# Kernel optimization log

Measured on AMD Instinct MI355X. Metric: run time of the kernel, lower is better.

Reference implementation:

```python
import jax, jax.numpy as jnp
import numpy as np

N = 10000      # nodes
E = 320000     # edges (before self-loops)
D_IN = 256
HID = 128
HEADS = 4
D_OUT = 256
SLOPE = 0.2    # PyG GATConv default negative_slope


def setup_inputs() -> dict:
    key = jax.random.key(0)
    ks = jax.random.split(key, 10)
    s = 0.05
    return {
        "x": jax.random.normal(ks[0], (N, D_IN), dtype=jnp.float32),
        "edge_index": jax.random.randint(ks[1], (2, E), 0, N),
        # layer 1: in=256 -> heads=4, out=128, concat
        "W1": jax.random.normal(ks[2], (D_IN, HEADS * HID), dtype=jnp.float32) * s,
        "a1_src": jax.random.normal(ks[3], (HEADS, HID), dtype=jnp.float32) * s,
        "a1_dst": jax.random.normal(ks[4], (HEADS, HID), dtype=jnp.float32) * s,
        "b1": jax.random.normal(ks[5], (HEADS * HID,), dtype=jnp.float32) * s,
        # layer 2: in=512 -> heads=1, out=256, no concat
        "W2": jax.random.normal(ks[6], (HEADS * HID, D_OUT), dtype=jnp.float32) * s,
        "a2_src": jax.random.normal(ks[7], (1, D_OUT), dtype=jnp.float32) * s,
        "a2_dst": jax.random.normal(ks[8], (1, D_OUT), dtype=jnp.float32) * s,
        "b2": jax.random.normal(ks[9], (D_OUT,), dtype=jnp.float32) * s,
    }


def gat_conv(x, src, dst, W, a_src, a_dst, bias, heads, out_dim, concat):
    """PyG-style GATConv (eval mode, self-loops pre-added to src/dst)."""
    n = x.shape[0]
    h = (x @ W).reshape(n, heads, out_dim)            # [N, H, F]
    # per-edge attention logits: LeakyReLU(a_src.h_src + a_dst.h_dst)
    as_n = (h * a_src).sum(-1)                         # [N, H]
    ad_n = (h * a_dst).sum(-1)                         # [N, H]
    logit = jax.nn.leaky_relu(as_n[src] + ad_n[dst], negative_slope=SLOPE)  # [E, H]
    # segment softmax over edges grouped by destination node
    logit = logit - jax.ops.segment_max(logit, dst, num_segments=n)[dst]
    ex = jnp.exp(logit)
    alpha = ex / jax.ops.segment_sum(ex, dst, num_segments=n)[dst]          # [E, H]
    # weighted scatter-aggregation of source messages
    out = jax.ops.segment_sum(h[src] * alpha[:, :, None], dst, num_segments=n)  # [N, H, F]
    out = out.reshape(n, heads * out_dim) if concat else out.mean(axis=1)
    return out + bias


def reference(x, edge_index, W1, a1_src, a1_dst, b1, W2, a2_src, a2_dst, b2):
    # add self-loops once (PyG GATConv default add_self_loops=True)
    loops = jnp.arange(N, dtype=edge_index.dtype)
    src = jnp.concatenate([edge_index[0], loops])
    dst = jnp.concatenate([edge_index[1], loops])
    h = gat_conv(x, src, dst, W1, a1_src, a1_dst, b1, HEADS, HID, True)
    h = jax.nn.elu(h)  # dropout is identity at eval
    return gat_conv(h, src, dst, W2, a2_src, a2_dst, b2, 1, D_OUT, False)
```

## Files before the change

### kernel.cpp

```cpp
#include <hip/hip_runtime.h>

#define N_NODES 10000
#define E_RAW   320000
#define E_TOT   330000
#define D_IN    256
#define HID     128
#define HEADS   4
#define F1      512
#define D_OUT   256
#define SLOPE   0.2f

typedef __attribute__((ext_vector_type(8))) short bf16x8;
typedef __attribute__((ext_vector_type(4))) float f32x4;

__device__ __forceinline__ float bf2f(ushort u) {
    return __uint_as_float(((uint)u) << 16);
}
__device__ __forceinline__ ushort f2bf(float x) {
    uint u = __float_as_uint(x);
    uint r = (u + 0x7FFFu + ((u >> 16) & 1u)) >> 16;
    return (ushort)r;
}
__device__ __forceinline__ float bfu_lo(uint u) { return __uint_as_float(u << 16); }
__device__ __forceinline__ float bfu_hi(uint u) { return __uint_as_float(u & 0xFFFF0000u); }

__device__ __forceinline__ void gload_lds16(const void* g, void* l) {
    __builtin_amdgcn_global_load_lds(
        (const __attribute__((address_space(1))) void*)g,
        (__attribute__((address_space(3))) void*)l, 16, 0, 0);
}


__global__ __launch_bounds__(256) void k_zero(int* __restrict__ p, int n) {
    int i = blockIdx.x * 256 + threadIdx.x;
    if (i < n) p[i] = 0;
}

__global__ __launch_bounds__(256) void k_hist(const int* __restrict__ ei, int* __restrict__ deg) {
    int e = blockIdx.x * 256 + threadIdx.x;
    if (e < E_TOT) {
        int dst = (e < E_RAW) ? ei[E_RAW + e] : (e - E_RAW);
        atomicAdd(&deg[dst], 1);
    }
}

#define SCAN_CHUNK 40

__global__ __launch_bounds__(256) void k_scan(const int* __restrict__ deg,
                                              int* __restrict__ row_start,
                                              int* __restrict__ cursor) {
    __shared__ int tots[256];
    int tid = threadIdx.x;
    int base = tid * SCAN_CHUNK;
    int loc[SCAN_CHUNK];
    int s = 0;
    #pragma unroll
    for (int k = 0; k < SCAN_CHUNK; k++) {
        int idx = base + k;
        int v = (idx < N_NODES) ? deg[idx] : 0;
        loc[k] = s;
        s += v;
    }
    tots[tid] = s;
    __syncthreads();
    for (int off = 1; off < 256; off <<= 1) {
        int t = (tid >= off) ? tots[tid - off] : 0;
        __syncthreads();
        tots[tid] += t;
        __syncthreads();
    }
    int excl = tots[tid] - s;
    #pragma unroll
    for (int k = 0; k < SCAN_CHUNK; k++) {
        int idx = base + k;
        if (idx < N_NODES) {
            int r = excl + loc[k];
            row_start[idx] = r;
            cursor[idx]    = r;
        }
    }
    if (tid == 255) row_start[N_NODES] = E_TOT;
}

__global__ __launch_bounds__(256) void k_scatter(const int* __restrict__ ei,
                                                 int* __restrict__ cursor,
                                                 int* __restrict__ csr_src) {
    int e = blockIdx.x * 256 + threadIdx.x;
    if (e < E_TOT) {
        int src = (e < E_RAW) ? ei[e] : (e - E_RAW);
        int dst = (e < E_RAW) ? ei[E_RAW + e] : (e - E_RAW);
        int pos = atomicAdd(&cursor[dst], 1);
        csr_src[pos] = src;
    }
}


__global__ __launch_bounds__(256) void k_cast8(const float* __restrict__ in,
                                               ushort* __restrict__ outp, int n8) {
    int i = blockIdx.x * 256 + threadIdx.x;
    if (i < n8) {
        float4 a = *(const float4*)&in[(size_t)i * 8];
        float4 b = *(const float4*)&in[(size_t)i * 8 + 4];
        uint4 u;
        u.x = (uint)f2bf(a.x) | ((uint)f2bf(a.y) << 16);
        u.y = (uint)f2bf(a.z) | ((uint)f2bf(a.w) << 16);
        u.z = (uint)f2bf(b.x) | ((uint)f2bf(b.y) << 16);
        u.w = (uint)f2bf(b.z) | ((uint)f2bf(b.w) << 16);
        *(uint4*)&outp[(size_t)i * 8] = u;
    }
}

__global__ __launch_bounds__(256) void k_castT(const float* __restrict__ in,
                                               ushort* __restrict__ outp,
                                               int K, int N) {
    int i = blockIdx.x * 256 + threadIdx.x;
    if (i < K * N) {
        int k = i / N, n = i - k * N;
        outp[(size_t)n * K + k] = f2bf(in[i]);
    }
}


__global__ __launch_bounds__(256) void k_gemm(const ushort* __restrict__ A,
                                              const ushort* __restrict__ B,
                                              ushort* __restrict__ C,
                                              int M, int N, int K) {
    __shared__ ushort sA[128 * 64];
    __shared__ ushort sB[64 * 64];

    const int tid = threadIdx.x;
    const int lane = tid & 63;
    const int wid = tid >> 6;
    const int wr = wid >> 1;
    const int wc = wid & 1;
    const int m0 = blockIdx.y * 128;
    const int n0 = blockIdx.x * 64;
    const int fr = lane & 15;
    const int fs = lane >> 4;

    const int rowc = lane >> 3;
    const int slot = (lane & 7) ^ rowc;

    f32x4 acc[4][2];
    #pragma unroll
    for (int i = 0; i < 4; i++)
        #pragma unroll
        for (int j = 0; j < 2; j++) acc[i][j] = (f32x4){0.f, 0.f, 0.f, 0.f};

    for (int k0 = 0; k0 < K; k0 += 64) {
        #pragma unroll
        for (int t = 0; t < 4; t++) {
            int c = wid + 4 * t;
            int gr = m0 + c * 8 + rowc;
            gr = gr < M ? gr : M - 1;
            gload_lds16(A + (size_t)gr * K + k0 + slot * 8, &sA[c * 512]);
        }
        #pragma unroll
        for (int t = 0; t < 2; t++) {
            int c = wid + 4 * t;
            int gc = n0 + c * 8 + rowc;
            gload_lds16(B + (size_t)gc * K + k0 + slot * 8, &sB[c * 512]);
        }
        __syncthreads();
        #pragma unroll
        for (int kk = 0; kk < 2; kk++) {
            int sbase = kk * 4 + fs;
            bf16x8 a_f[4], b_f[2];
            #pragma unroll
            for (int i = 0; i < 4; i++) {
                int r = wr * 64 + i * 16 + fr;
                a_f[i] = *(const bf16x8*)&sA[r * 64 + ((sbase ^ (r & 7)) << 3)];
            }
            #pragma unroll
            for (int j = 0; j < 2; j++) {
                int cc = wc * 32 + j * 16 + fr;
                b_f[j] = *(const bf16x8*)&sB[cc * 64 + ((sbase ^ (cc & 7)) << 3)];
            }
            #pragma unroll
            for (int i = 0; i < 4; i++)
                #pragma unroll
                for (int j = 0; j < 2; j++)
                    acc[i][j] = __builtin_amdgcn_mfma_f32_16x16x32_bf16(a_f[i], b_f[j], acc[i][j], 0, 0, 0);
        }
        __syncthreads();
    }

    #pragma unroll
    for (int i = 0; i < 4; i++) {
        #pragma unroll
        for (int j = 0; j < 2; j++) {
            int row_base = m0 + wr * 64 + i * 16 + ((lane >> 4) << 2);
            int col = n0 + wc * 32 + j * 16 + (lane & 15);
            #pragma unroll
            for (int q = 0; q < 4; q++) {
                int r = row_base + q;
                if (r < M) C[(size_t)r * N + col] = f2bf(acc[i][j][q]);
            }
        }
    }
}


__global__ __launch_bounds__(256) void k_attn_vec1(const ushort* __restrict__ h1,
                                                   const float* __restrict__ a1s,
                                                   const float* __restrict__ a1d,
                                                   float* __restrict__ as1,
                                                   float* __restrict__ ad1) {
    int node = blockIdx.x * 4 + (threadIdx.x >> 6);
    int lane = threadIdx.x & 63;
    uint4 hv = *(const uint4*)(h1 + (size_t)node * F1 + (size_t)lane * 8);
    const float* sp = a1s + lane * 8;
    const float* dp = a1d + lane * 8;
    float4 sa = *(const float4*)sp, sb = *(const float4*)(sp + 4);
    float4 da = *(const float4*)dp, db = *(const float4*)(dp + 4);
    float h0 = bfu_lo(hv.x), h1v = bfu_hi(hv.x), h2v = bfu_lo(hv.y), h3 = bfu_hi(hv.y);
    float h4 = bfu_lo(hv.z), h5 = bfu_hi(hv.z), h6 = bfu_lo(hv.w), h7 = bfu_hi(hv.w);
    float s_ = h0*sa.x + h1v*sa.y + h2v*sa.z + h3*sa.w + h4*sb.x + h5*sb.y + h6*sb.z + h7*sb.w;
    float d_ = h0*da.x + h1v*da.y + h2v*da.z + h3*da.w + h4*db.x + h5*db.y + h6*db.z + h7*db.w;
    #pragma unroll
    for (int off = 8; off >= 1; off >>= 1) {
        s_ += __shfl_xor(s_, off, 64);
        d_ += __shfl_xor(d_, off, 64);
    }
    if ((lane & 15) == 0) {
        int head = lane >> 4;
        as1[node * 4 + head] = s_;
        ad1[node * 4 + head] = d_;
    }
}

__global__ __launch_bounds__(256) void k_attn_vec2(const ushort* __restrict__ h2,
                                                   const float* __restrict__ a2s,
                                                   const float* __restrict__ a2d,
                                                   float* __restrict__ as2,
                                                   float* __restrict__ ad2) {
    int node = blockIdx.x * 4 + (threadIdx.x >> 6);
    int lane = threadIdx.x & 63;
    uint2 hv = *(const uint2*)(h2 + (size_t)node * D_OUT + lane * 4);
    float h0 = bfu_lo(hv.x), h1v = bfu_hi(hv.x), h2v = bfu_lo(hv.y), h3 = bfu_hi(hv.y);
    float4 sv = *(const float4*)(a2s + lane * 4);
    float4 dv = *(const float4*)(a2d + lane * 4);
    float s_ = h0 * sv.x + h1v * sv.y + h2v * sv.z + h3 * sv.w;
    float d_ = h0 * dv.x + h1v * dv.y + h2v * dv.z + h3 * dv.w;
    #pragma unroll
    for (int off = 32; off >= 1; off >>= 1) {
        s_ += __shfl_xor(s_, off, 64);
        d_ += __shfl_xor(d_, off, 64);
    }
    if (lane == 0) { as2[node] = s_; ad2[node] = d_; }
}


__device__ __forceinline__ void fma8(uint4 v, float e, float* acc) {
    acc[0] += bfu_lo(v.x) * e; acc[1] += bfu_hi(v.x) * e;
    acc[2] += bfu_lo(v.y) * e; acc[3] += bfu_hi(v.y) * e;
    acc[4] += bfu_lo(v.z) * e; acc[5] += bfu_hi(v.z) * e;
    acc[6] += bfu_lo(v.w) * e; acc[7] += bfu_hi(v.w) * e;
}

__global__ __launch_bounds__(256) void k_edge1(const int* __restrict__ row_start,
                                               const int* __restrict__ csr_src,
                                               const ushort* __restrict__ h1,
                                               const float* __restrict__ as1,
                                               const float* __restrict__ ad1,
                                               const float* __restrict__ b1,
                                               ushort* __restrict__ heluh) {
    int node = blockIdx.x * 4 + (threadIdx.x >> 6);
    int lane = threadIdx.x & 63;
    int start = row_start[node];
    int end   = row_start[node + 1];
    int h_lane = lane >> 4;

    float adl = ad1[node * 4 + h_lane];

    float acc[8] = {0,0,0,0,0,0,0,0};
    float sum = 0.f;
    const size_t lo8 = (size_t)lane * 8;

    int i = start;
    for (; i + 8 <= end; i += 8) {
        int s[8];
        #pragma unroll
        for (int k = 0; k < 8; k++) s[k] = csr_src[i + k];
        float l[8];
        #pragma unroll
        for (int k = 0; k < 8; k++) l[k] = as1[s[k] * 4 + h_lane];
        uint4 v[8];
        #pragma unroll
        for (int k = 0; k < 8; k++) v[k] = *(const uint4*)(h1 + (size_t)s[k] * F1 + lo8);
        #pragma unroll
        for (int k = 0; k < 8; k++) {
            float t = l[k] + adl;
            t = t > 0.f ? t : SLOPE * t;
            float e = __expf(t);
            sum += e;
            fma8(v[k], e, acc);
        }
    }
    for (; i < end; i++) {
        int s0 = csr_src[i];
        float t = as1[s0 * 4 + h_lane] + adl;
        uint4 v0 = *(const uint4*)(h1 + (size_t)s0 * F1 + lo8);
        t = t > 0.f ? t : SLOPE * t;
        float e = __expf(t);
        sum += e;
        fma8(v0, e, acc);
    }
    float inv = 1.f / sum;

    size_t o = (size_t)node * F1 + lo8;
    const float* bp = b1 + lo8;
    uint pk[4];
    #pragma unroll
    for (int j = 0; j < 4; j++) {
        float v0 = acc[2*j]   * inv + bp[2*j];
        float v1 = acc[2*j+1] * inv + bp[2*j+1];
        v0 = v0 > 0.f ? v0 : (__expf(v0) - 1.f);
        v1 = v1 > 0.f ? v1 : (__expf(v1) - 1.f);
        pk[j] = (uint)f2bf(v0) | ((uint)f2bf(v1) << 16);
    }
    *(uint4*)&heluh[o] = make_uint4(pk[0], pk[1], pk[2], pk[3]);
}

__global__ __launch_bounds__(256) void k_edge2(const int* __restrict__ row_start,
                                               const int* __restrict__ csr_src,
                                               const ushort* __restrict__ h2,
                                               const float* __restrict__ as2,
                                               const float* __restrict__ ad2,
                                               const float* __restrict__ b2,
                                               float* __restrict__ out) {
    int node = blockIdx.x * 4 + (threadIdx.x >> 6);
    int lane = threadIdx.x & 63;
    int start = row_start[node];
    int end   = row_start[node + 1];

    float ad = ad2[node];

    float acc[4] = {0,0,0,0};
    float sum = 0.f;
    const size_t lo4 = (size_t)lane * 4;

    int i = start;
    for (; i + 8 <= end; i += 8) {
        int s[8];
        #pragma unroll
        for (int k = 0; k < 8; k++) s[k] = csr_src[i + k];
        float l[8];
        #pragma unroll
        for (int k = 0; k < 8; k++) l[k] = as2[s[k]];
        uint2 v[8];
        #pragma unroll
        for (int k = 0; k < 8; k++) v[k] = *(const uint2*)(h2 + (size_t)s[k] * D_OUT + lo4);
        #pragma unroll
        for (int k = 0; k < 8; k++) {
            float t = l[k] + ad;
            t = t > 0.f ? t : SLOPE * t;
            float e = __expf(t);
            sum += e;
            acc[0] += bfu_lo(v[k].x) * e; acc[1] += bfu_hi(v[k].x) * e;
            acc[2] += bfu_lo(v[k].y) * e; acc[3] += bfu_hi(v[k].y) * e;
        }
    }
    for (; i < end; i++) {
        int s0 = csr_src[i];
        float t = as2[s0] + ad;
        uint2 v0 = *(const uint2*)(h2 + (size_t)s0 * D_OUT + lo4);
        t = t > 0.f ? t : SLOPE * t;
        float e = __expf(t);
        sum += e;
        acc[0] += bfu_lo(v0.x) * e; acc[1] += bfu_hi(v0.x) * e;
        acc[2] += bfu_lo(v0.y) * e; acc[3] += bfu_hi(v0.y) * e;
    }
    float inv = 1.f / sum;
    float4 r;
    r.x = acc[0] * inv + b2[lo4 + 0];
    r.y = acc[1] * inv + b2[lo4 + 1];
    r.z = acc[2] * inv + b2[lo4 + 2];
    r.w = acc[3] * inv + b2[lo4 + 3];
    *(float4*)&out[(size_t)node * D_OUT + lo4] = r;
}


extern "C" void kernel_launch(void* const* d_in, const int* in_sizes, int n_in,
                              void* d_out, int out_size, void* d_ws, size_t ws_size,
                              hipStream_t stream) {
    const float* x   = (const float*)d_in[0];
    const int*   ei  = (const int*)d_in[1];
    const float* W1  = (const float*)d_in[2];
    const float* a1s = (const float*)d_in[3];
    const float* a1d = (const float*)d_in[4];
    const float* b1  = (const float*)d_in[5];
    const float* W2  = (const float*)d_in[6];
    const float* a2s = (const float*)d_in[7];
    const float* a2d = (const float*)d_in[8];
    const float* b2  = (const float*)d_in[9];
    float* out = (float*)d_out;

    char* ws = (char*)d_ws;
    size_t off = 0;
    auto take = [&](size_t bytes) {
        char* p = ws + off;
        off += (bytes + 255) & ~(size_t)255;
        return p;
    };
    int*    deg       = (int*)take(sizeof(int) * N_NODES);
    int*    row_start = (int*)take(sizeof(int) * (N_NODES + 1));
    int*    cursor    = (int*)take(sizeof(int) * N_NODES);
    int*    csr_src   = (int*)take(sizeof(int) * E_TOT);
    ushort* xb        = (ushort*)take(sizeof(ushort) * (size_t)N_NODES * D_IN);
    ushort* w1h       = (ushort*)take(sizeof(ushort) * D_IN * F1);
    ushort* w2h       = (ushort*)take(sizeof(ushort) * F1 * D_OUT);
    ushort* h1        = (ushort*)take(sizeof(ushort) * (size_t)N_NODES * F1);
    float*  as1       = (float*)take(sizeof(float) * N_NODES * 4);
    float*  ad1       = (float*)take(sizeof(float) * N_NODES * 4);
    ushort* heluh     = (ushort*)take(sizeof(ushort) * (size_t)N_NODES * F1);
    ushort* h2        = (ushort*)take(sizeof(ushort) * (size_t)N_NODES * D_OUT);
    float*  as2       = (float*)take(sizeof(float) * N_NODES);
    float*  ad2       = (float*)take(sizeof(float) * N_NODES);

    int eblocks = (E_TOT + 255) / 256;
    k_zero<<<(N_NODES + 255) / 256, 256, 0, stream>>>(deg, N_NODES);
    k_hist<<<eblocks, 256, 0, stream>>>(ei, deg);
    k_scan<<<1, 256, 0, stream>>>(deg, row_start, cursor);
    k_scatter<<<eblocks, 256, 0, stream>>>(ei, cursor, csr_src);

    k_cast8<<<(N_NODES * D_IN / 8 + 255) / 256, 256, 0, stream>>>(x, xb, N_NODES * D_IN / 8);
    k_castT<<<(D_IN * F1 + 255) / 256, 256, 0, stream>>>(W1, w1h, D_IN, F1);
    k_castT<<<(F1 * D_OUT + 255) / 256, 256, 0, stream>>>(W2, w2h, F1, D_OUT);

    k_gemm<<<dim3(F1 / 64, (N_NODES + 127) / 128), 256, 0, stream>>>(xb, w1h, h1, N_NODES, F1, D_IN);
    k_attn_vec1<<<N_NODES / 4, 256, 0, stream>>>(h1, a1s, a1d, as1, ad1);
    k_edge1<<<N_NODES / 4, 256, 0, stream>>>(row_start, csr_src, h1, as1, ad1, b1, heluh);

    k_gemm<<<dim3(D_OUT / 64, (N_NODES + 127) / 128), 256, 0, stream>>>(heluh, w2h, h2, N_NODES, D_OUT, F1);
    k_attn_vec2<<<N_NODES / 4, 256, 0, stream>>>(h2, a2s, a2d, as2, ad2);
    k_edge2<<<N_NODES / 4, 256, 0, stream>>>(row_start, csr_src, h2, as2, ad2, b2, out);
}
```

Baseline: 168.1 us.

## Fuse attention-vector dots into GEMM epilogues and merge prep kernels

Computes the per-node attention dot products in the GEMM epilogues with shuffle reductions and atomicAdd, which removes the separate attn_vec kernels and their re-read of h1/h2. The scan and all casts go into one multi-role prep kernel, and the CSR scatter shares a launch with GEMM1 blocks. k_edge2 now has each half-wave take alternate edges with 16-byte loads. Together these cut the launch count, at the cost of extra zeroing and atomic traffic and a float summation order that is no longer deterministic.

```diff
diff --git a/kernel.cpp b/kernel.cpp
--- a/kernel.cpp
+++ b/kernel.cpp
@@ -9,6 +9,7 @@
 #define F1      512
 #define D_OUT   256
 #define SLOPE   0.2f
+#define EBLOCKS 1290
 
 typedef __attribute__((ext_vector_type(8))) short bf16x8;
 typedef __attribute__((ext_vector_type(4))) float f32x4;
@@ -31,10 +32,16 @@
 }
 
 
-__global__ __launch_bounds__(256) void k_zero(int* __restrict__ p, int n) {
+__global__ __launch_bounds__(256) void k_zero_all(int* __restrict__ deg,
+                                                  float* __restrict__ as1,
+                                                  float* __restrict__ ad1,
+                                                  float* __restrict__ as2,
+                                                  float* __restrict__ ad2) {
     int i = blockIdx.x * 256 + threadIdx.x;
-    if (i < n) p[i] = 0;
-}
+    if (i < 4 * N_NODES) { as1[i] = 0.f; ad1[i] = 0.f; }
+    if (i < N_NODES) { deg[i] = 0; as2[i] = 0.f; ad2[i] = 0.f; }
+}
+
 
 __global__ __launch_bounds__(256) void k_hist(const int* __restrict__ ei, int* __restrict__ deg) {
     int e = blockIdx.x * 256 + threadIdx.x;
@@ -44,210 +51,227 @@
     }
 }
 
+
 #define SCAN_CHUNK 40
 
-__global__ __launch_bounds__(256) void k_scan(const int* __restrict__ deg,
+__global__ __launch_bounds__(256) void k_prep(const int* __restrict__ deg,
                                               int* __restrict__ row_start,
-                                              int* __restrict__ cursor) {
-    __shared__ int tots[256];
+                                              int* __restrict__ cursor,
+                                              const float* __restrict__ W1,
+                                              ushort* __restrict__ w1h,
+                                              const float* __restrict__ W2,
+                                              ushort* __restrict__ w2h,
+                                              const float* __restrict__ x,
+                                              ushort* __restrict__ xb) {
+    int b = blockIdx.x;
     int tid = threadIdx.x;
-    int base = tid * SCAN_CHUNK;
-    int loc[SCAN_CHUNK];
-    int s = 0;
-    #pragma unroll
-    for (int k = 0; k < SCAN_CHUNK; k++) {
-        int idx = base + k;
-        int v = (idx < N_NODES) ? deg[idx] : 0;
-        loc[k] = s;
-        s += v;
-    }
-    tots[tid] = s;
-    __syncthreads();
-    for (int off = 1; off < 256; off <<= 1) {
-        int t = (tid >= off) ? tots[tid - off] : 0;
+    if (b == 0) {
+        __shared__ int tots[256];
+        int base = tid * SCAN_CHUNK;
+        int loc[SCAN_CHUNK];
+        int s = 0;
+        #pragma unroll
+        for (int k = 0; k < SCAN_CHUNK; k++) {
+            int idx = base + k;
+            int v = (idx < N_NODES) ? deg[idx] : 0;
+            loc[k] = s;
+            s += v;
+        }
+        tots[tid] = s;
         __syncthreads();
-        tots[tid] += t;
-        __syncthreads();
-    }
-    int excl = tots[tid] - s;
-    #pragma unroll
-    for (int k = 0; k < SCAN_CHUNK; k++) {
-        int idx = base + k;
-        if (idx < N_NODES) {
-            int r = excl + loc[k];
-            row_start[idx] = r;
-            cursor[idx]    = r;
-        }
-    }
-    if (tid == 255) row_start[N_NODES] = E_TOT;
-}
-
-__global__ __launch_bounds__(256) void k_scatter(const int* __restrict__ ei,
-                                                 int* __restrict__ cursor,
-                                                 int* __restrict__ csr_src) {
-    int e = blockIdx.x * 256 + threadIdx.x;
-    if (e < E_TOT) {
-        int src = (e < E_RAW) ? ei[e] : (e - E_RAW);
-        int dst = (e < E_RAW) ? ei[E_RAW + e] : (e - E_RAW);
-        int pos = atomicAdd(&cursor[dst], 1);
-        csr_src[pos] = src;
-    }
-}
-
-
-__global__ __launch_bounds__(256) void k_cast8(const float* __restrict__ in,
-                                               ushort* __restrict__ outp, int n8) {
-    int i = blockIdx.x * 256 + threadIdx.x;
-    if (i < n8) {
-        float4 a = *(const float4*)&in[(size_t)i * 8];
-        float4 b = *(const float4*)&in[(size_t)i * 8 + 4];
+        for (int off = 1; off < 256; off <<= 1) {
+            int t = (tid >= off) ? tots[tid - off] : 0;
+            __syncthreads();
+            tots[tid] += t;
+            __syncthreads();
+        }
+        int excl = tots[tid] - s;
+        #pragma unroll
+        for (int k = 0; k < SCAN_CHUNK; k++) {
+            int idx = base + k;
+            if (idx < N_NODES) {
+                int r = excl + loc[k];
+                row_start[idx] = r;
+                cursor[idx]    = r;
+            }
+        }
+        if (tid == 255) row_start[N_NODES] = E_TOT;
+    } else if (b <= 512) {
+        int i = (b - 1) * 256 + tid;
+        int k = i / F1, n = i - k * F1;
+        w1h[(size_t)n * D_IN + k] = f2bf(W1[i]);
+    } else if (b <= 1024) {
+        int i = (b - 513) * 256 + tid;
+        int k = i / D_OUT, n = i - k * D_OUT;
+        w2h[(size_t)n * F1 + k] = f2bf(W2[i]);
+    } else {
+        int i8 = (b - 1025) * 256 + tid;
+        float4 a = *(const float4*)&x[(size_t)i8 * 8];
+        float4 c = *(const float4*)&x[(size_t)i8 * 8 + 4];
         uint4 u;
         u.x = (uint)f2bf(a.x) | ((uint)f2bf(a.y) << 16);
         u.y = (uint)f2bf(a.z) | ((uint)f2bf(a.w) << 16);
-        u.z = (uint)f2bf(b.x) | ((uint)f2bf(b.y) << 16);
-        u.w = (uint)f2bf(b.z) | ((uint)f2bf(b.w) << 16);
-        *(uint4*)&outp[(size_t)i * 8] = u;
-    }
-}
-
-__global__ __launch_bounds__(256) void k_castT(const float* __restrict__ in,
-                                               ushort* __restrict__ outp,
-                                               int K, int N) {
-    int i = blockIdx.x * 256 + threadIdx.x;
-    if (i < K * N) {
-        int k = i / N, n = i - k * N;
-        outp[(size_t)n * K + k] = f2bf(in[i]);
-    }
-}
-
-
-__global__ __launch_bounds__(256) void k_gemm(const ushort* __restrict__ A,
-                                              const ushort* __restrict__ B,
-                                              ushort* __restrict__ C,
-                                              int M, int N, int K) {
-    __shared__ ushort sA[128 * 64];
+        u.z = (uint)f2bf(c.x) | ((uint)f2bf(c.y) << 16);
+        u.w = (uint)f2bf(c.z) | ((uint)f2bf(c.w) << 16);
+        *(uint4*)&xb[(size_t)i8 * 8] = u;
+    }
+}
+
+
+template<int BM, int KD, int ND, int WC, int HMUL>
+__device__ __forceinline__ void gemm_attn(int bx, int by, int tid,
+                                          const ushort* __restrict__ A,
+                                          const ushort* __restrict__ B,
+                                          ushort* __restrict__ C,
+                                          const float* __restrict__ avs,
+                                          const float* __restrict__ avd,
+                                          float* __restrict__ os,
+                                          float* __restrict__ od) {
+    constexpr int WR = 4 / WC;
+    constexpr int MI = (BM / WR) / 16;
+    constexpr int NJ = (64 / WC) / 16;
+    __shared__ ushort sA[BM * 64];
     __shared__ ushort sB[64 * 64];
 
-    const int tid = threadIdx.x;
     const int lane = tid & 63;
     const int wid = tid >> 6;
-    const int wr = wid >> 1;
-    const int wc = wid & 1;
-    const int m0 = blockIdx.y * 128;
-    const int n0 = blockIdx.x * 64;
+    const int wr = wid / WC;
+    const int wc = wid % WC;
+    const int m0 = by * BM;
+    const int n0 = bx * 64;
     const int fr = lane & 15;
     const int fs = lane >> 4;
-
     const int rowc = lane >> 3;
     const int slot = (lane & 7) ^ rowc;
 
-    f32x4 acc[4][2];
+    f32x4 acc[MI][NJ];
     #pragma unroll
-    for (int i = 0; i < 4; i++)
-        #pragma unroll
-        for (int j = 0; j < 2; j++) acc[i][j] = (f32x4){0.f, 0.f, 0.f, 0.f};
-
-    for (int k0 = 0; k0 < K; k0 += 64) {
-        #pragma unroll
-        for (int t = 0; t < 4; t++) {
+    for (int i = 0; i < MI; i++)
+        #pragma unroll
+        for (int j = 0; j < NJ; j++) acc[i][j] = (f32x4){0.f, 0.f, 0.f, 0.f};
+
+    for (int k0 = 0; k0 < KD; k0 += 64) {
+        #pragma unroll
+        for (int t = 0; t < BM / 32; t++) {
             int c = wid + 4 * t;
             int gr = m0 + c * 8 + rowc;
-            gr = gr < M ? gr : M - 1;
-            gload_lds16(A + (size_t)gr * K + k0 + slot * 8, &sA[c * 512]);
+            gr = gr < N_NODES ? gr : N_NODES - 1;
+            gload_lds16(A + (size_t)gr * KD + k0 + slot * 8, &sA[c * 512]);
         }
         #pragma unroll
         for (int t = 0; t < 2; t++) {
             int c = wid + 4 * t;
-            int gc = n0 + c * 8 + rowc;
-            gload_lds16(B + (size_t)gc * K + k0 + slot * 8, &sB[c * 512]);
+            gload_lds16(B + (size_t)(n0 + c * 8 + rowc) * KD + k0 + slot * 8, &sB[c * 512]);
         }
         __syncthreads();
         #pragma unroll
         for (int kk = 0; kk < 2; kk++) {
             int sbase = kk * 4 + fs;
-            bf16x8 a_f[4], b_f[2];
-            #pragma unroll
-            for (int i = 0; i < 4; i++) {
+            bf16x8 a_f[MI], b_f[NJ];
+            #pragma unroll
+            for (int i = 0; i < MI; i++) {
                 int r = wr * 64 + i * 16 + fr;
                 a_f[i] = *(const bf16x8*)&sA[r * 64 + ((sbase ^ (r & 7)) << 3)];
             }
             #pragma unroll
-            for (int j = 0; j < 2; j++) {
-                int cc = wc * 32 + j * 16 + fr;
+            for (int j = 0; j < NJ; j++) {
+                int cc = wc * (64 / WC) + j * 16 + fr;
                 b_f[j] = *(const bf16x8*)&sB[cc * 64 + ((sbase ^ (cc & 7)) << 3)];
             }
             #pragma unroll
-            for (int i = 0; i < 4; i++)
+            for (int i = 0; i < MI; i++)
                 #pragma unroll
-                for (int j = 0; j < 2; j++)
+                for (int j = 0; j < NJ; j++)
                     acc[i][j] = __builtin_amdgcn_mfma_f32_16x16x32_bf16(a_f[i], b_f[j], acc[i][j], 0, 0, 0);
         }
         __syncthreads();
     }
 
+    const int hoff = (HMUL == 4) ? (n0 >> 7) : 0;
+    float sv[NJ], dv[NJ];
+    int cols[NJ];
     #pragma unroll
-    for (int i = 0; i < 4; i++) {
-        #pragma unroll
-        for (int j = 0; j < 2; j++) {
-            int row_base = m0 + wr * 64 + i * 16 + ((lane >> 4) << 2);
-            int col = n0 + wc * 32 + j * 16 + (lane & 15);
+    for (int j = 0; j < NJ; j++) {
+        cols[j] = n0 + wc * (64 / WC) + j * 16 + fr;
+        sv[j] = avs[cols[j]];
+        dv[j] = avd[cols[j]];
+    }
+    #pragma unroll
+    for (int i = 0; i < MI; i++) {
+        int row_base = m0 + wr * 64 + i * 16 + (fs << 2);
+        float ps[4], pd[4];
+        #pragma unroll
+        for (int q = 0; q < 4; q++) {
+            int r = row_base + q;
+            float p_s = 0.f, p_d = 0.f;
+            #pragma unroll
+            for (int j = 0; j < NJ; j++) {
+                float v = acc[i][j][q];
+                if (r < N_NODES) C[(size_t)r * ND + cols[j]] = f2bf(v);
+                p_s += v * sv[j];
+                p_d += v * dv[j];
+            }
+            ps[q] = p_s; pd[q] = p_d;
+        }
+        #pragma unroll
+        for (int q = 0; q < 4; q++) {
+            #pragma unroll
+            for (int m = 8; m >= 1; m >>= 1) {
+                ps[q] += __shfl_xor(ps[q], m, 16);
+                pd[q] += __shfl_xor(pd[q], m, 16);
+            }
+        }
+        if (fr == 0) {
             #pragma unroll
             for (int q = 0; q < 4; q++) {
                 int r = row_base + q;
-                if (r < M) C[(size_t)r * N + col] = f2bf(acc[i][j][q]);
-            }
-        }
-    }
-}
-
-
-__global__ __launch_bounds__(256) void k_attn_vec1(const ushort* __restrict__ h1,
-                                                   const float* __restrict__ a1s,
-                                                   const float* __restrict__ a1d,
-                                                   float* __restrict__ as1,
-                                                   float* __restrict__ ad1) {
-    int node = blockIdx.x * 4 + (threadIdx.x >> 6);
-    int lane = threadIdx.x & 63;
-    uint4 hv = *(const uint4*)(h1 + (size_t)node * F1 + (size_t)lane * 8);
-    const float* sp = a1s + lane * 8;
-    const float* dp = a1d + lane * 8;
-    float4 sa = *(const float4*)sp, sb = *(const float4*)(sp + 4);
-    float4 da = *(const float4*)dp, db = *(const float4*)(dp + 4);
-    float h0 = bfu_lo(hv.x), h1v = bfu_hi(hv.x), h2v = bfu_lo(hv.y), h3 = bfu_hi(hv.y);
-    float h4 = bfu_lo(hv.z), h5 = bfu_hi(hv.z), h6 = bfu_lo(hv.w), h7 = bfu_hi(hv.w);
-    float s_ = h0*sa.x + h1v*sa.y + h2v*sa.z + h3*sa.w + h4*sb.x + h5*sb.y + h6*sb.z + h7*sb.w;
-    float d_ = h0*da.x + h1v*da.y + h2v*da.z + h3*da.w + h4*db.x + h5*db.y + h6*db.z + h7*db.w;
-    #pragma unroll
-    for (int off = 8; off >= 1; off >>= 1) {
-        s_ += __shfl_xor(s_, off, 64);
-        d_ += __shfl_xor(d_, off, 64);
-    }
-    if ((lane & 15) == 0) {
-        int head = lane >> 4;
-        as1[node * 4 + head] = s_;
-        ad1[node * 4 + head] = d_;
-    }
-}
-
-__global__ __launch_bounds__(256) void k_attn_vec2(const ushort* __restrict__ h2,
-                                                   const float* __restrict__ a2s,
-                                                   const float* __restrict__ a2d,
-                                                   float* __restrict__ as2,
-                                                   float* __restrict__ ad2) {
-    int node = blockIdx.x * 4 + (threadIdx.x >> 6);
-    int lane = threadIdx.x & 63;
-    uint2 hv = *(const uint2*)(h2 + (size_t)node * D_OUT + lane * 4);
-    float h0 = bfu_lo(hv.x), h1v = bfu_hi(hv.x), h2v = bfu_lo(hv.y), h3 = bfu_hi(hv.y);
-    float4 sv = *(const float4*)(a2s + lane * 4);
-    float4 dv = *(const float4*)(a2d + lane * 4);
-    float s_ = h0 * sv.x + h1v * sv.y + h2v * sv.z + h3 * sv.w;
-    float d_ = h0 * dv.x + h1v * dv.y + h2v * dv.z + h3 * dv.w;
-    #pragma unroll
-    for (int off = 32; off >= 1; off >>= 1) {
-        s_ += __shfl_xor(s_, off, 64);
-        d_ += __shfl_xor(d_, off, 64);
-    }
-    if (lane == 0) { as2[node] = s_; ad2[node] = d_; }
+                if (r < N_NODES) {
+                    atomicAdd(&os[r * HMUL + hoff], ps[q]);
+                    atomicAdd(&od[r * HMUL + hoff], pd[q]);
+                }
+            }
+        }
+    }
+}
+
+
+__global__ __launch_bounds__(256) void k_mid(const int* __restrict__ ei,
+                                             int* __restrict__ cursor,
+                                             int* __restrict__ csr_src,
+                                             const ushort* __restrict__ xb,
+                                             const ushort* __restrict__ w1h,
+                                             ushort* __restrict__ h1,
+                                             const float* __restrict__ a1s,
+                                             const float* __restrict__ a1d,
+                                             float* __restrict__ as1,
+                                             float* __restrict__ ad1) {
+    int b = blockIdx.x;
+    if (b < EBLOCKS) {
+        int e = b * 256 + threadIdx.x;
+        if (e < E_TOT) {
+            int src = (e < E_RAW) ? ei[e] : (e - E_RAW);
+            int dst = (e < E_RAW) ? ei[E_RAW + e] : (e - E_RAW);
+            int pos = atomicAdd(&cursor[dst], 1);
+            csr_src[pos] = src;
+        }
+        return;
+    }
+    int g = b - EBLOCKS;
+    gemm_attn<128, D_IN, F1, 2, 4>(g % 8, g / 8, threadIdx.x,
+                                   xb, w1h, h1, a1s, a1d, as1, ad1);
+}
+
+
+__global__ __launch_bounds__(256) void k_gemm2(const ushort* __restrict__ heluh,
+                                               const ushort* __restrict__ w2h,
+                                               ushort* __restrict__ h2,
+                                               const float* __restrict__ a2s,
+                                               const float* __restrict__ a2d,
+                                               float* __restrict__ as2,
+                                               float* __restrict__ ad2) {
+    int b = blockIdx.x;
+    gemm_attn<64, F1, D_OUT, 4, 1>(b % 4, b / 4, threadIdx.x,
+                                   heluh, w2h, h2, a2s, a2d, as2, ad2);
 }
 
 
@@ -331,53 +355,64 @@
                                                float* __restrict__ out) {
     int node = blockIdx.x * 4 + (threadIdx.x >> 6);
     int lane = threadIdx.x & 63;
+    int sub = lane >> 5;
+    int fl  = lane & 31;
     int start = row_start[node];
     int end   = row_start[node + 1];
 
     float ad = ad2[node];
 
-    float acc[4] = {0,0,0,0};
+    float acc[8] = {0,0,0,0,0,0,0,0};
     float sum = 0.f;
-    const size_t lo4 = (size_t)lane * 4;
+    const size_t fo = (size_t)fl * 8;
 
     int i = start;
     for (; i + 8 <= end; i += 8) {
-        int s[8];
-        #pragma unroll
-        for (int k = 0; k < 8; k++) s[k] = csr_src[i + k];
-        float l[8];
-        #pragma unroll
-        for (int k = 0; k < 8; k++) l[k] = as2[s[k]];
-        uint2 v[8];
-        #pragma unroll
-        for (int k = 0; k < 8; k++) v[k] = *(const uint2*)(h2 + (size_t)s[k] * D_OUT + lo4);
-        #pragma unroll
-        for (int k = 0; k < 8; k++) {
+        int s[4];
+        #pragma unroll
+        for (int k = 0; k < 4; k++) s[k] = csr_src[i + 2 * k + sub];
+        float l[4];
+        #pragma unroll
+        for (int k = 0; k < 4; k++) l[k] = as2[s[k]];
+        uint4 v[4];
+        #pragma unroll
+        for (int k = 0; k < 4; k++) v[k] = *(const uint4*)(h2 + (size_t)s[k] * D_OUT + fo);
+        #pragma unroll
+        for (int k = 0; k < 4; k++) {
             float t = l[k] + ad;
             t = t > 0.f ? t : SLOPE * t;
             float e = __expf(t);
             sum += e;
-            acc[0] += bfu_lo(v[k].x) * e; acc[1] += bfu_hi(v[k].x) * e;
-            acc[2] += bfu_lo(v[k].y) * e; acc[3] += bfu_hi(v[k].y) * e;
-        }
-    }
-    for (; i < end; i++) {
-        int s0 = csr_src[i];
-        float t = as2[s0] + ad;
-        uint2 v0 = *(const uint2*)(h2 + (size_t)s0 * D_OUT + lo4);
-        t = t > 0.f ? t : SLOPE * t;
-        float e = __expf(t);
-        sum += e;
-        acc[0] += bfu_lo(v0.x) * e; acc[1] += bfu_hi(v0.x) * e;
-        acc[2] += bfu_lo(v0.y) * e; acc[3] += bfu_hi(v0.y) * e;
-    }
+            fma8(v[k], e, acc);
+        }
+    }
+    for (; i < end; i += 2) {
+        if (i + sub < end) {
+            int s0 = csr_src[i + sub];
+            float t = as2[s0] + ad;
+            uint4 v0 = *(const uint4*)(h2 + (size_t)s0 * D_OUT + fo);
+            t = t > 0.f ? t : SLOPE * t;
+            float e = __expf(t);
+            sum += e;
+            fma8(v0, e, acc);
+        }
+    }
+    #pragma unroll
+    for (int j = 0; j < 8; j++) acc[j] += __shfl_xor(acc[j], 32, 64);
+    sum += __shfl_xor(sum, 32, 64);
     float inv = 1.f / sum;
-    float4 r;
-    r.x = acc[0] * inv + b2[lo4 + 0];
-    r.y = acc[1] * inv + b2[lo4 + 1];
-    r.z = acc[2] * inv + b2[lo4 + 2];
-    r.w = acc[3] * inv + b2[lo4 + 3];
-    *(float4*)&out[(size_t)node * D_OUT + lo4] = r;
+
+    if (lane < 32) {
+        size_t o = (size_t)node * D_OUT + fo;
+        const float* bp = b2 + fo;
+        float4 r0, r1;
+        r0.x = acc[0] * inv + bp[0]; r0.y = acc[1] * inv + bp[1];
+        r0.z = acc[2] * inv + bp[2]; r0.w = acc[3] * inv + bp[3];
+        r1.x = acc[4] * inv + bp[4]; r1.y = acc[5] * inv + bp[5];
+        r1.z = acc[6] * inv + bp[6]; r1.w = acc[7] * inv + bp[7];
+        *(float4*)&out[o] = r0;
+        *(float4*)&out[o + 4] = r1;
+    }
 }
 
 
@@ -418,21 +453,12 @@
     float*  as2       = (float*)take(sizeof(float) * N_NODES);
     float*  ad2       = (float*)take(sizeof(float) * N_NODES);
 
-    int eblocks = (E_TOT + 255) / 256;
-    k_zero<<<(N_NODES + 255) / 256, 256, 0, stream>>>(deg, N_NODES);
-    k_hist<<<eblocks, 256, 0, stream>>>(ei, deg);
-    k_scan<<<1, 256, 0, stream>>>(deg, row_start, cursor);
-    k_scatter<<<eblocks, 256, 0, stream>>>(ei, cursor, csr_src);
-
-    k_cast8<<<(N_NODES * D_IN / 8 + 255) / 256, 256, 0, stream>>>(x, xb, N_NODES * D_IN / 8);
-    k_castT<<<(D_IN * F1 + 255) / 256, 256, 0, stream>>>(W1, w1h, D_IN, F1);
-    k_castT<<<(F1 * D_OUT + 255) / 256, 256, 0, stream>>>(W2, w2h, F1, D_OUT);
-
-    k_gemm<<<dim3(F1 / 64, (N_NODES + 127) / 128), 256, 0, stream>>>(xb, w1h, h1, N_NODES, F1, D_IN);
-    k_attn_vec1<<<N_NODES / 4, 256, 0, stream>>>(h1, a1s, a1d, as1, ad1);
+    k_zero_all<<<(4 * N_NODES + 255) / 256, 256, 0, stream>>>(deg, as1, ad1, as2, ad2);
+    k_hist<<<EBLOCKS, 256, 0, stream>>>(ei, deg);
+    k_prep<<<2275, 256, 0, stream>>>(deg, row_start, cursor, W1, w1h, W2, w2h, x, xb);
+    k_mid<<<EBLOCKS + 8 * 79, 256, 0, stream>>>(ei, cursor, csr_src, xb, w1h, h1,
+                                                a1s, a1d, as1, ad1);
     k_edge1<<<N_NODES / 4, 256, 0, stream>>>(row_start, csr_src, h1, as1, ad1, b1, heluh);
-
-    k_gemm<<<dim3(D_OUT / 64, (N_NODES + 127) / 128), 256, 0, stream>>>(heluh, w2h, h2, N_NODES, D_OUT, F1);
-    k_attn_vec2<<<N_NODES / 4, 256, 0, stream>>>(h2, a2s, a2d, as2, ad2);
+    k_gemm2<<<4 * 157, 256, 0, stream>>>(heluh, w2h, h2, a2s, a2d, as2, ad2);
     k_edge2<<<N_NODES / 4, 256, 0, stream>>>(row_start, csr_src, h2, as2, ad2, b2, out);
 }
```

Result: no change. 169.9 us (+1.1%).
